# Kernel optimization log

Hardware: AMD Instinct MI355X
Metric: run time of the kernel (lower is better)

## Reference

```python
import jax, jax.numpy as jnp
import numpy as np

M, K, N = 8192, 4096, 4096

def setup_inputs() -> dict:
    key = jax.random.key(0)
    k1, k2, k3, k4, k5 = jax.random.split(key, 5)
    # int8-range quantized tensors stored as int32 (int8 values in [-128, 127])
    inp = jax.random.randint(k1, (M, K), -128, 128, dtype=jnp.int32)
    weight = jax.random.randint(k2, (N, K), -128, 128, dtype=jnp.int32)
    bias = jax.random.normal(k3, (N,), dtype=jnp.float32)
    inp_scales = jax.random.uniform(k4, (1,), jnp.float32, 0.01, 0.05)        # per-tensor
    inp_zero_points = jnp.zeros((1,), jnp.int32)                               # symmetric
    weight_scales = jax.random.uniform(k5, (N,), jnp.float32, 0.005, 0.02)     # per-channel
    weight_zero_points = jnp.zeros((N,), jnp.int32)
    return {
        "inp": inp, "weight": weight, "bias": bias,
        "inp_scales": inp_scales, "inp_zero_points": inp_zero_points,
        "weight_scales": weight_scales, "weight_zero_points": weight_zero_points,
    }

def reference(inp, weight, bias, inp_scales, inp_zero_points, weight_scales, weight_zero_points):
    # qdq_linear fallback path: dequantize activation (per-tensor) and weight
    # (per-output-channel), fp32 matmul, add bias. output_dtype=float32,
    # output_scales/zero_points=None => no output requantization.
    x = (inp.astype(jnp.float32) - inp_zero_points.astype(jnp.float32)) * inp_scales  # [M,K]
    w = (weight.astype(jnp.float32) - weight_zero_points[:, None].astype(jnp.float32)) \
        * weight_scales[:, None]                                                      # [N,K]
    return jnp.einsum('mk,nk->mn', x, w) + bias                                       # [M,N]
```

## Files before the change

### kernel.cpp

```cpp
#include <hip/hip_runtime.h>

#define MM 8192
#define NN 4096
#define KK 4096

#define BM 128
#define BN 128
#define BK 128

typedef int int32x4 __attribute__((ext_vector_type(4)));

__device__ __forceinline__ void async_load16(const void* g, void* l) {
  __builtin_amdgcn_global_load_lds(
      (__attribute__((address_space(1))) void*)(void*)g,
      (__attribute__((address_space(3))) void*)l,
      16, 0, 0);
}

__global__ __launch_bounds__(256) void pack_kernel(
    const int* __restrict__ a, const int* __restrict__ w,
    char* __restrict__ a8, char* __restrict__ w8,
    const int* __restrict__ izp, const int* __restrict__ wzp) {
  const long tid = (long)blockIdx.x * 256 + threadIdx.x;
  const long A_T = (long)MM * KK / 4;

  const int4* src;
  int* dst;
  int z;
  if (tid < A_T) {
    src = (const int4*)a + tid;
    dst = (int*)a8 + tid;
    z = izp[0];
  } else {
    long t = tid - A_T;
    src = (const int4*)w + t;
    dst = (int*)w8 + t;
    z = wzp[t >> 10];
  }

  int4 v = *src;
  union { char c[4]; int q; } u;
  u.c[0] = (char)(v.x - z);
  u.c[1] = (char)(v.y - z);
  u.c[2] = (char)(v.z - z);
  u.c[3] = (char)(v.w - z);
  *dst = u.q;
}

__global__ __launch_bounds__(256, 2) void qgemm_kernel(
    const char* __restrict__ A8, const char* __restrict__ W8,
    float* __restrict__ out,
    const float* __restrict__ bias,
    const float* __restrict__ is_ptr,
    const float* __restrict__ wscale) {
  __shared__ __attribute__((aligned(16))) char As[BM * BK];
  __shared__ __attribute__((aligned(16))) char Bs[BN * BK];

  int pid = blockIdx.x;
  pid = (pid & 7) * 256 + (pid >> 3);
  const int group  = pid >> 8;
  const int within = pid & 255;
  const int bm = group * 8 + (within & 7);
  const int bn = within >> 3;

  const int tid  = threadIdx.x;
  const int wave = tid >> 6;
  const int lane = tid & 63;
  const int wm = (wave >> 1) * 64;
  const int wn = (wave & 1) * 64;

  const int srow = lane >> 3;
  const int ssub = (lane & 7) ^ srow;
  const char* a_src[4];
  const char* b_src[4];
  char* a_dst[4];
  char* b_dst[4];
#pragma unroll
  for (int j = 0; j < 4; ++j) {
    const int c = wave + j * 4;
    a_src[j] = A8 + (long)(bm * BM + c * 8 + srow) * KK + ssub * 16;
    b_src[j] = W8 + (long)(bn * BN + c * 8 + srow) * KK + ssub * 16;
    a_dst[j] = As + c * 1024;
    b_dst[j] = Bs + c * 1024;
  }

  const int row_q = lane & 15;
  const int quad  = lane >> 4;
  const int psub0 = quad ^ (row_q & 7);
  const int psub1 = psub0 ^ 4;
  const char* a_rd = As + (wm + row_q) * BK;
  const char* b_rd = Bs + (wn + row_q) * BK;

  int32x4 acc[4][4];
#pragma unroll
  for (int mi = 0; mi < 4; ++mi)
#pragma unroll
    for (int ni = 0; ni < 4; ++ni) acc[mi][ni] = (int32x4)0;

  for (int kk = 0; kk < KK; kk += BK) {
#pragma unroll
    for (int j = 0; j < 4; ++j) {
      async_load16(a_src[j] + kk, a_dst[j]);
      async_load16(b_src[j] + kk, b_dst[j]);
    }
    __syncthreads();

#pragma unroll
    for (int h = 0; h < 2; ++h) {
      const int ps = (h == 0) ? psub0 : psub1;
      int32x4 afrag[4], bfrag[4];
#pragma unroll
      for (int mi = 0; mi < 4; ++mi)
        afrag[mi] = *(const int32x4*)(a_rd + mi * 16 * BK + ps * 16);
#pragma unroll
      for (int ni = 0; ni < 4; ++ni)
        bfrag[ni] = *(const int32x4*)(b_rd + ni * 16 * BK + ps * 16);

#pragma unroll
      for (int mi = 0; mi < 4; ++mi)
#pragma unroll
        for (int ni = 0; ni < 4; ++ni)
          acc[mi][ni] = __builtin_amdgcn_mfma_i32_16x16x64_i8(
              afrag[mi], bfrag[ni], acc[mi][ni], 0, 0, 0);
    }

    __syncthreads();
  }

  const float is0 = is_ptr[0];
  const int row_base = bm * BM + wm + quad * 4;
  const int col_base = bn * BN + wn + row_q;
#pragma unroll
  for (int ni = 0; ni < 4; ++ni) {
    const int col = col_base + ni * 16;
    const float s = is0 * wscale[col];
    const float b = bias[col];
#pragma unroll
    for (int mi = 0; mi < 4; ++mi) {
      const int row = row_base + mi * 16;
#pragma unroll
      for (int r = 0; r < 4; ++r) {
        out[(long)(row + r) * NN + col] = (float)acc[mi][ni][r] * s + b;
      }
    }
  }
}

extern "C" void kernel_launch(void* const* d_in, const int* in_sizes, int n_in,
                              void* d_out, int out_size, void* d_ws, size_t ws_size,
                              hipStream_t stream) {
  const int*   inp    = (const int*)d_in[0];
  const int*   weight = (const int*)d_in[1];
  const float* bias   = (const float*)d_in[2];
  const float* iscale = (const float*)d_in[3];
  const int*   izp    = (const int*)d_in[4];
  const float* wscale = (const float*)d_in[5];
  const int*   wzp    = (const int*)d_in[6];
  float* out = (float*)d_out;

  char* a8 = (char*)d_ws;
  char* w8 = a8 + (size_t)MM * KK;

  pack_kernel<<<49152, 256, 0, stream>>>(inp, weight, a8, w8, izp, wzp);

  qgemm_kernel<<<2048, 256, 0, stream>>>(a8, w8, out, bias, iscale, wscale);
}
```

Baseline: 391.6 us.

## Double-buffer int8 GEMM with 256x256 tiles, 32x32 MFMA, and wider pack stores

The GEMM now uses 256x256 block tiles with 512 threads and double-buffered LDS. The next K-tile is loaded asynchronously in four phases interleaved with compute, and s_setprio and barriers control the schedule. Compute switches from 16x16x64 to 32x32x32 int8 MFMA, and the epilogue row mapping is changed to match. The pack kernel writes 16 bytes per thread instead of 4. The intent is to hide global-load latency and raise data reuse per block, at the cost of 128KB of LDS and only 512 blocks, which risks low occupancy and a tail effect.

Result: slower. 413.5 us (+5.6%).

```diff
diff --git a/kernel.cpp b/kernel.cpp
--- a/kernel.cpp
+++ b/kernel.cpp
@@ -4,11 +4,15 @@
 #define NN 4096
 #define KK 4096
 
-#define BM 128
-#define BN 128
+#define BM 256
+#define BN 256
 #define BK 128
-
-typedef int int32x4 __attribute__((ext_vector_type(4)));
+#define NT (KK / BK)
+#define ABUF (BM * BK)
+#define BBUF (BN * BK)
+
+typedef int int32x4  __attribute__((ext_vector_type(4)));
+typedef int int32x16 __attribute__((ext_vector_type(16)));
 
 __device__ __forceinline__ void async_load16(const void* g, void* l) {
   __builtin_amdgcn_global_load_lds(
@@ -22,128 +26,157 @@
     char* __restrict__ a8, char* __restrict__ w8,
     const int* __restrict__ izp, const int* __restrict__ wzp) {
   const long tid = (long)blockIdx.x * 256 + threadIdx.x;
-  const long A_T = (long)MM * KK / 4;
+  const long A_T = (long)MM * KK / 16;
 
   const int4* src;
-  int* dst;
+  int4* dst;
   int z;
   if (tid < A_T) {
-    src = (const int4*)a + tid;
-    dst = (int*)a8 + tid;
+    src = (const int4*)a + tid * 4;
+    dst = (int4*)a8 + tid;
     z = izp[0];
   } else {
-    long t = tid - A_T;
-    src = (const int4*)w + t;
-    dst = (int*)w8 + t;
-    z = wzp[t >> 10];
-  }
-
-  int4 v = *src;
-  union { char c[4]; int q; } u;
-  u.c[0] = (char)(v.x - z);
-  u.c[1] = (char)(v.y - z);
-  u.c[2] = (char)(v.z - z);
-  u.c[3] = (char)(v.w - z);
+    const long t = tid - A_T;
+    src = (const int4*)w + t * 4;
+    dst = (int4*)w8 + t;
+    z = wzp[t >> 8];
+  }
+
+  int4 v0 = src[0], v1 = src[1], v2 = src[2], v3 = src[3];
+  union { char c[16]; int4 q; } u;
+  u.c[0]  = (char)(v0.x - z); u.c[1]  = (char)(v0.y - z);
+  u.c[2]  = (char)(v0.z - z); u.c[3]  = (char)(v0.w - z);
+  u.c[4]  = (char)(v1.x - z); u.c[5]  = (char)(v1.y - z);
+  u.c[6]  = (char)(v1.z - z); u.c[7]  = (char)(v1.w - z);
+  u.c[8]  = (char)(v2.x - z); u.c[9]  = (char)(v2.y - z);
+  u.c[10] = (char)(v2.z - z); u.c[11] = (char)(v2.w - z);
+  u.c[12] = (char)(v3.x - z); u.c[13] = (char)(v3.y - z);
+  u.c[14] = (char)(v3.z - z); u.c[15] = (char)(v3.w - z);
   *dst = u.q;
 }
 
-__global__ __launch_bounds__(256, 2) void qgemm_kernel(
+__global__ __launch_bounds__(512, 2) void qgemm_kernel(
     const char* __restrict__ A8, const char* __restrict__ W8,
     float* __restrict__ out,
     const float* __restrict__ bias,
     const float* __restrict__ is_ptr,
     const float* __restrict__ wscale) {
-  __shared__ __attribute__((aligned(16))) char As[BM * BK];
-  __shared__ __attribute__((aligned(16))) char Bs[BN * BK];
+  __shared__ __attribute__((aligned(16))) char As[2 * ABUF];
+  __shared__ __attribute__((aligned(16))) char Bs[2 * BBUF];
 
   int pid = blockIdx.x;
-  pid = (pid & 7) * 256 + (pid >> 3);
-  const int group  = pid >> 8;
-  const int within = pid & 255;
-  const int bm = group * 8 + (within & 7);
-  const int bn = within >> 3;
+  pid = (pid & 7) * 64 + (pid >> 3);
+  const int bm = pid >> 4;
+  const int bn = pid & 15;
 
   const int tid  = threadIdx.x;
-  const int wave = tid >> 6;
+  const int wid  = tid >> 6;
   const int lane = tid & 63;
-  const int wm = (wave >> 1) * 64;
-  const int wn = (wave & 1) * 64;
+  const int wm = (wid >> 2) * 128;
+  const int wn = (wid & 3) * 64;
 
   const int srow = lane >> 3;
-  const int ssub = (lane & 7) ^ srow;
+  const int ssub = (lane & 7) ^ (srow & 7);
   const char* a_src[4];
   const char* b_src[4];
-  char* a_dst[4];
-  char* b_dst[4];
-#pragma unroll
-  for (int j = 0; j < 4; ++j) {
-    const int c = wave + j * 4;
-    a_src[j] = A8 + (long)(bm * BM + c * 8 + srow) * KK + ssub * 16;
-    b_src[j] = W8 + (long)(bn * BN + c * 8 + srow) * KK + ssub * 16;
-    a_dst[j] = As + c * 1024;
-    b_dst[j] = Bs + c * 1024;
-  }
-
-  const int row_q = lane & 15;
-  const int quad  = lane >> 4;
-  const int psub0 = quad ^ (row_q & 7);
-  const int psub1 = psub0 ^ 4;
-  const char* a_rd = As + (wm + row_q) * BK;
-  const char* b_rd = Bs + (wn + row_q) * BK;
-
-  int32x4 acc[4][4];
+  int a_off[4];
+#pragma unroll
+  for (int i = 0; i < 4; ++i) {
+    const int c = wid + i * 8;
+    a_src[i] = A8 + (long)(bm * BM + c * 8 + srow) * KK + ssub * 16;
+    b_src[i] = W8 + (long)(bn * BN + c * 8 + srow) * KK + ssub * 16;
+    a_off[i] = c * 1024;
+  }
+
+#define STAGE_A(I, T) \
+  async_load16(a_src[I] + (T) * BK, As + ((T) & 1) * ABUF + a_off[I])
+#define STAGE_B(I, T) \
+  async_load16(b_src[I] + (T) * BK, Bs + ((T) & 1) * BBUF + a_off[I])
+
+  const int r31 = lane & 31;
+  const int hi  = lane >> 5;
+  const int l7  = lane & 7;
+  const char* a_rd = As + (wm + r31) * BK;
+  const char* b_rd = Bs + (wn + r31) * BK;
+  const int ps0 = (((0 + hi) ^ l7) * 16);
+  const int ps1 = (((2 + hi) ^ l7) * 16);
+  const int ps2 = (((4 + hi) ^ l7) * 16);
+  const int ps3 = (((6 + hi) ^ l7) * 16);
+
+  int32x16 acc[4][2];
 #pragma unroll
   for (int mi = 0; mi < 4; ++mi)
 #pragma unroll
-    for (int ni = 0; ni < 4; ++ni) acc[mi][ni] = (int32x4)0;
-
-  for (int kk = 0; kk < KK; kk += BK) {
-#pragma unroll
-    for (int j = 0; j < 4; ++j) {
-      async_load16(a_src[j] + kk, a_dst[j]);
-      async_load16(b_src[j] + kk, b_dst[j]);
-    }
-    __syncthreads();
-
-#pragma unroll
-    for (int h = 0; h < 2; ++h) {
-      const int ps = (h == 0) ? psub0 : psub1;
-      int32x4 afrag[4], bfrag[4];
-#pragma unroll
-      for (int mi = 0; mi < 4; ++mi)
-        afrag[mi] = *(const int32x4*)(a_rd + mi * 16 * BK + ps * 16);
-#pragma unroll
-      for (int ni = 0; ni < 4; ++ni)
-        bfrag[ni] = *(const int32x4*)(b_rd + ni * 16 * BK + ps * 16);
-
-#pragma unroll
-      for (int mi = 0; mi < 4; ++mi)
-#pragma unroll
-        for (int ni = 0; ni < 4; ++ni)
-          acc[mi][ni] = __builtin_amdgcn_mfma_i32_16x16x64_i8(
-              afrag[mi], bfrag[ni], acc[mi][ni], 0, 0, 0);
-    }
-
-    __syncthreads();
+    for (int ni = 0; ni < 2; ++ni) acc[mi][ni] = (int32x16)0;
+
+#pragma unroll
+  for (int i = 0; i < 4; ++i) STAGE_A(i, 0);
+#pragma unroll
+  for (int i = 0; i < 4; ++i) STAGE_B(i, 0);
+  STAGE_A(0, 1);
+  STAGE_A(1, 1);
+  asm volatile("s_waitcnt vmcnt(2)" ::: "memory");
+  __builtin_amdgcn_s_barrier();
+
+#define PHASE(PS, CUR, STAGE_STMT)                                          \
+  {                                                                         \
+    const char* ar_ = a_rd + (CUR) * ABUF;                                  \
+    const char* br_ = b_rd + (CUR) * BBUF;                                  \
+    int32x4 af0 = *(const int32x4*)(ar_ + 0 * 32 * BK + (PS));              \
+    int32x4 af1 = *(const int32x4*)(ar_ + 1 * 32 * BK + (PS));              \
+    int32x4 af2 = *(const int32x4*)(ar_ + 2 * 32 * BK + (PS));              \
+    int32x4 af3 = *(const int32x4*)(ar_ + 3 * 32 * BK + (PS));              \
+    int32x4 bf0 = *(const int32x4*)(br_ + 0 * 32 * BK + (PS));              \
+    int32x4 bf1 = *(const int32x4*)(br_ + 1 * 32 * BK + (PS));              \
+    STAGE_STMT;                                                             \
+    __builtin_amdgcn_s_barrier();                                           \
+    __builtin_amdgcn_s_setprio(1);                                          \
+    acc[0][0] = __builtin_amdgcn_mfma_i32_32x32x32_i8(af0, bf0, acc[0][0], 0, 0, 0); \
+    acc[0][1] = __builtin_amdgcn_mfma_i32_32x32x32_i8(af0, bf1, acc[0][1], 0, 0, 0); \
+    acc[1][0] = __builtin_amdgcn_mfma_i32_32x32x32_i8(af1, bf0, acc[1][0], 0, 0, 0); \
+    acc[1][1] = __builtin_amdgcn_mfma_i32_32x32x32_i8(af1, bf1, acc[1][1], 0, 0, 0); \
+    acc[2][0] = __builtin_amdgcn_mfma_i32_32x32x32_i8(af2, bf0, acc[2][0], 0, 0, 0); \
+    acc[2][1] = __builtin_amdgcn_mfma_i32_32x32x32_i8(af2, bf1, acc[2][1], 0, 0, 0); \
+    acc[3][0] = __builtin_amdgcn_mfma_i32_32x32x32_i8(af3, bf0, acc[3][0], 0, 0, 0); \
+    acc[3][1] = __builtin_amdgcn_mfma_i32_32x32x32_i8(af3, bf1, acc[3][1], 0, 0, 0); \
+    __builtin_amdgcn_s_setprio(0);                                          \
+  }
+
+#pragma unroll 2
+  for (int t = 0; t < NT; ++t) {
+    const int cur = t & 1;
+    PHASE(ps0, cur, if (t + 1 < NT) { STAGE_A(2, t + 1); STAGE_A(3, t + 1); })
+    __builtin_amdgcn_s_barrier();
+    PHASE(ps1, cur, if (t + 1 < NT) { STAGE_B(0, t + 1); STAGE_B(1, t + 1); })
+    __builtin_amdgcn_s_barrier();
+    PHASE(ps2, cur, if (t + 1 < NT) { STAGE_B(2, t + 1); STAGE_B(3, t + 1); })
+    __builtin_amdgcn_s_barrier();
+    PHASE(ps3, cur, if (t + 2 < NT) { STAGE_A(0, t + 2); STAGE_A(1, t + 2); })
+    asm volatile("s_waitcnt vmcnt(2)" ::: "memory");
+    __builtin_amdgcn_s_barrier();
   }
 
   const float is0 = is_ptr[0];
-  const int row_base = bm * BM + wm + quad * 4;
-  const int col_base = bn * BN + wn + row_q;
-#pragma unroll
-  for (int ni = 0; ni < 4; ++ni) {
-    const int col = col_base + ni * 16;
+  const int row_base = bm * BM + wm + 4 * hi;
+  const int col_base = bn * BN + wn + r31;
+#pragma unroll
+  for (int ni = 0; ni < 2; ++ni) {
+    const int col = col_base + ni * 32;
     const float s = is0 * wscale[col];
     const float b = bias[col];
 #pragma unroll
     for (int mi = 0; mi < 4; ++mi) {
-      const int row = row_base + mi * 16;
-#pragma unroll
-      for (int r = 0; r < 4; ++r) {
-        out[(long)(row + r) * NN + col] = (float)acc[mi][ni][r] * s + b;
+      const long rb = (long)(row_base + mi * 32) * NN + col;
+#pragma unroll
+      for (int r = 0; r < 16; ++r) {
+        const int roff = (r & 3) + 8 * (r >> 2);
+        out[rb + (long)roff * NN] = (float)acc[mi][ni][r] * s + b;
       }
     }
   }
+#undef PHASE
+#undef STAGE_A
+#undef STAGE_B
 }
 
 extern "C" void kernel_launch(void* const* d_in, const int* in_sizes, int n_in,
@@ -161,7 +194,7 @@
   char* a8 = (char*)d_ws;
   char* w8 = a8 + (size_t)MM * KK;
 
-  pack_kernel<<<49152, 256, 0, stream>>>(inp, weight, a8, w8, izp, wzp);
-
-  qgemm_kernel<<<2048, 256, 0, stream>>>(a8, w8, out, bias, iscale, wscale);
-}
+  pack_kernel<<<12288, 256, 0, stream>>>(inp, weight, a8, w8, izp, wzp);
+
+  qgemm_kernel<<<512, 512, 0, stream>>>(a8, w8, out, bias, iscale, wscale);
+}
```
